# Optimization experiments

Hardware: AMD Instinct MI355X
Metric: run time of the kernel (lower is better)

The kernel has to match this reference:

```python
import jax, jax.numpy as jnp
import numpy as np

N = 50000
E = 1600000
D_IN = 128
HID = 64
OUT = 64
NEG_SLOPE = 0.2


def _glorot(key, shape):
    fan_in = shape[0]
    return jax.random.normal(key, shape, dtype=jnp.float32) / np.sqrt(fan_in)


def _layer_params(key, din, dout):
    ks = jax.random.split(key, 4)
    return dict(
        Wl=_glorot(ks[0], (din, dout)), bl=jnp.zeros((dout,), jnp.float32),
        Wr=_glorot(ks[1], (din, dout)), br=jnp.zeros((dout,), jnp.float32),
        We=_glorot(ks[2], (1, dout)),
        att=jax.random.normal(ks[3], (dout,), dtype=jnp.float32) / np.sqrt(dout),
        b=jnp.zeros((dout,), jnp.float32),
    )


def setup_inputs() -> dict:
    key = jax.random.key(0)
    kx, ke, ka, k0, k1, k2 = jax.random.split(key, 6)
    x = jax.random.normal(kx, (N, D_IN), dtype=jnp.float32)
    edge_index = jax.random.randint(ke, (2, E), 0, N, dtype=jnp.int64)
    edge_attr = jax.random.uniform(ka, (E, 1), dtype=jnp.float32)
    p0 = _layer_params(k0, D_IN, HID)
    p1 = _layer_params(k1, HID, HID)
    p2 = _layer_params(k2, HID, OUT)
    inp = {"x": x, "edge_index": edge_index, "edge_attr": edge_attr}
    for i, p in enumerate((p0, p1, p2)):
        for name, v in p.items():
            inp[f"{name}{i}"] = v
    return inp


def gatv2_layer(x, src, dst, edge_attr, Wl, bl, Wr, br, We, att, b):
    # GATv2Conv, heads=1, no self loops, edge_dim=1
    xl = x @ Wl + bl                      # [N, C] source transform
    xr = x @ Wr + br                      # [N, C] target transform
    m = xl[src] + xr[dst] + edge_attr @ We  # [E, C]
    m = jnp.where(m > 0, m, NEG_SLOPE * m)  # leaky_relu(0.2)
    logits = m @ att                      # [E]
    # segment softmax over destination nodes
    lmax = jax.ops.segment_max(logits, dst, num_segments=N)
    lmax = jnp.where(jnp.isfinite(lmax), lmax, 0.0)
    ex = jnp.exp(logits - lmax[dst])
    denom = jax.ops.segment_sum(ex, dst, num_segments=N)
    alpha = ex / (denom[dst] + 1e-16)     # [E]
    out = jax.ops.segment_sum(xl[src] * alpha[:, None], dst, num_segments=N)
    return out + b


def reference(x, edge_index, edge_attr,
              Wl0, bl0, Wr0, br0, We0, att0, b0,
              Wl1, bl1, Wr1, br1, We1, att1, b1,
              Wl2, bl2, Wr2, br2, We2, att2, b2):
    src, dst = edge_index[0], edge_index[1]
    h = gatv2_layer(x, src, dst, edge_attr, Wl0, bl0, Wr0, br0, We0, att0, b0)
    h = jax.nn.relu(h)
    h = gatv2_layer(h, src, dst, edge_attr, Wl1, bl1, Wr1, br1, We1, att1, b1)
    h = jax.nn.relu(h)
    h = gatv2_layer(h, src, dst, edge_attr, Wl2, bl2, Wr2, br2, We2, att2, b2)
    # final_activation=False
    return h
```

## Files before the change

### kernel.cpp

```cpp
#include <hip/hip_runtime.h>
#include <math.h>


#define NEG_SLOPE 0.2f

__global__ __launch_bounds__(256) void kA_hist(
    const int* __restrict__ dst, int E, int nbuck, int chunk,
    int* __restrict__ blockhist )
{
    __shared__ int h[256];
    int tid = threadIdx.x, blk = blockIdx.x, nblk = gridDim.x;
    for (int i = tid; i < nbuck; i += 256) h[i] = 0;
    __syncthreads();
    int s0 = blk * chunk, s1 = min(s0 + chunk, E);
    for (int e = s0 + tid; e < s1; e += 256)
        atomicAdd(&h[dst[e] >> 8], 1);
    __syncthreads();
    for (int i = tid; i < nbuck; i += 256)
        blockhist[i * nblk + blk] = h[i];
}

__global__ __launch_bounds__(1024) void k_scan(const int* __restrict__ counts, int n,
                                               int* __restrict__ offsets) {
    __shared__ int wsum[16];
    __shared__ int wpre[16];
    __shared__ int chunktot;
    int tid = threadIdx.x;
    int lane = tid & 63;
    int w = tid >> 6;
    int carry = 0;
    for (int base = 0; base < n; base += 1024) {
        int i = base + tid;
        int v = (i < n) ? counts[i] : 0;
        int incl = v;
        #pragma unroll
        for (int off = 1; off < 64; off <<= 1) {
            int t = __shfl_up(incl, off, 64);
            if (lane >= off) incl += t;
        }
        if (lane == 63) wsum[w] = incl;
        __syncthreads();
        if (tid == 0) {
            int acc = 0;
            #pragma unroll
            for (int j = 0; j < 16; ++j) { int t = wsum[j]; wpre[j] = acc; acc += t; }
            chunktot = acc;
        }
        __syncthreads();
        int excl = incl - v + wpre[w] + carry;
        if (i < n) offsets[i] = excl;
        carry += chunktot;
        __syncthreads();
    }
    if (tid == 0) offsets[n] = carry;
}

__global__ __launch_bounds__(256) void kA_scatter(
    const int* __restrict__ src, const int* __restrict__ dst,
    const float* __restrict__ ea, int E, int nbuck, int chunk, int nblk,
    const int* __restrict__ cursA, int2* __restrict__ tmp)
{
    __shared__ int cur[256];
    int tid = threadIdx.x, blk = blockIdx.x;
    for (int i = tid; i < nbuck; i += 256) cur[i] = cursA[i * nblk + blk];
    __syncthreads();
    int s0 = blk * chunk, s1 = min(s0 + chunk, E);
    for (int e = s0 + tid; e < s1; e += 256) {
        int d = dst[e];
        int pos = atomicAdd(&cur[d >> 8], 1);
        tmp[pos] = make_int2((d << 16) | src[e], __float_as_int(ea[e]));
    }
}

__global__ __launch_bounds__(256) void kB_sort(
    const int2* __restrict__ tmp, const int* __restrict__ cursA,
    int nblk, int E, int n,
    int2* __restrict__ srec, int* __restrict__ offsets)
{
    __shared__ int h[256];
    __shared__ int cur2[256];
    int b = blockIdx.x, tid = threadIdx.x;
    int start = cursA[b * nblk];
    int end   = cursA[(b + 1) * nblk];
    h[tid] = 0;
    __syncthreads();
    for (int e = start + tid; e < end; e += 256)
        atomicAdd(&h[(tmp[e].x >> 16) & 255], 1);
    __syncthreads();
    if (tid == 0) {
        int acc = start;
        for (int i = 0; i < 256; ++i) { int c = h[i]; cur2[i] = acc; acc += c; }
    }
    __syncthreads();
    int v = (b << 8) + tid;
    if (v < n) offsets[v] = cur2[tid];
    if (b == 0 && tid == 0) offsets[n] = E;
    __syncthreads();
    for (int e = start + tid; e < end; e += 256) {
        int2 r = tmp[e];
        int pos = atomicAdd(&cur2[(r.x >> 16) & 255], 1);
        srec[pos] = make_int2(r.x & 0xFFFF, r.y);
    }
}

template<int DIN>
__global__ __launch_bounds__(256) void k_linear(
    const float* __restrict__ x,
    const float* __restrict__ Wl, const float* __restrict__ bl,
    const float* __restrict__ Wr, const float* __restrict__ br,
    float* __restrict__ xl, float* __restrict__ xr, int n)
{
    __shared__ float sWl[DIN * 64];
    __shared__ float sWr[DIN * 64];
    __shared__ float sX[16 * DIN];
    int tid = threadIdx.x;
    for (int i = tid * 4; i < DIN * 64; i += 256 * 4) {
        *(float4*)&sWl[i] = *(const float4*)&Wl[i];
        *(float4*)&sWr[i] = *(const float4*)&Wr[i];
    }
    int nb = blockIdx.x * 16;
    int totx = n * DIN;
    for (int i = tid * 4; i < 16 * DIN; i += 256 * 4) {
        int g = nb * DIN + i;
        if (g < totx) *(float4*)&sX[i] = *(const float4*)&x[g];
    }
    __syncthreads();
    int lane = tid & 63;
    int grp = tid >> 6;
    float blv = bl[lane], brv = br[lane];
    float accL[4], accR[4];
    #pragma unroll
    for (int j = 0; j < 4; ++j) { accL[j] = blv; accR[j] = brv; }
    const float* sx0 = &sX[(grp * 4) * DIN];
    #pragma unroll 4
    for (int k = 0; k < DIN; ++k) {
        float wl = sWl[k * 64 + lane];
        float wr = sWr[k * 64 + lane];
        #pragma unroll
        for (int j = 0; j < 4; ++j) {
            float xk = sx0[j * DIN + k];
            accL[j] += xk * wl;
            accR[j] += xk * wr;
        }
    }
    #pragma unroll
    for (int j = 0; j < 4; ++j) {
        int node = nb + grp * 4 + j;
        if (node < n) {
            xl[node * 64 + lane] = accL[j];
            xr[node * 64 + lane] = accR[j];
        }
    }
}

__global__ __launch_bounds__(256) void k_edge(
    const float* __restrict__ xl, const float* __restrict__ xr,
    const int2* __restrict__ srec,
    const int* __restrict__ offsets,
    const float* __restrict__ We, const float* __restrict__ att,
    const float* __restrict__ b,
    float* __restrict__ out, int n, int relu)
{
    int wave = threadIdx.x >> 6;
    int lane = threadIdx.x & 63;
    int v = blockIdx.x * 4 + wave;
    if (v >= n) return;
    int start = offsets[v];
    int end   = offsets[v + 1];
    float xr_c  = xr[v * 64 + lane];
    float We_c  = We[lane];
    float att_c = att[lane];
    float M = -INFINITY, S = 0.f, O = 0.f;

    for (int e = start; e < end; e += 8) {
        int cnt = end - e;
        int2 rec[8]; float xlc[8], p[8];
        #pragma unroll
        for (int i = 0; i < 8; ++i) {
            int ii = (i < cnt) ? i : 0;
            rec[i] = srec[e + ii];
        }
        #pragma unroll
        for (int i = 0; i < 8; ++i) xlc[i] = xl[rec[i].x * 64 + lane];
        #pragma unroll
        for (int i = 0; i < 8; ++i) {
            float m = xlc[i] + xr_c + __int_as_float(rec[i].y) * We_c;
            m = m > 0.f ? m : NEG_SLOPE * m;
            p[i] = (i < cnt) ? m * att_c : -INFINITY;
        }
        float q[4];
        #pragma unroll
        for (int i = 0; i < 4; ++i) {
            float a = p[2*i]   + __shfl_xor(p[2*i],   1, 64);
            float c = p[2*i+1] + __shfl_xor(p[2*i+1], 1, 64);
            q[i] = (lane & 1) ? c : a;
        }
        float r[2];
        #pragma unroll
        for (int i = 0; i < 2; ++i) {
            float a = q[2*i]   + __shfl_xor(q[2*i],   2, 64);
            float c = q[2*i+1] + __shfl_xor(q[2*i+1], 2, 64);
            r[i] = (lane & 2) ? c : a;
        }
        float s_;
        {
            float a = r[0] + __shfl_xor(r[0], 4, 64);
            float c = r[1] + __shfl_xor(r[1], 4, 64);
            s_ = (lane & 4) ? c : a;
        }
        s_ += __shfl_xor(s_, 8, 64);
        s_ += __shfl_xor(s_, 16, 64);
        s_ += __shfl_xor(s_, 32, 64);

        float bm = s_;
        bm = fmaxf(bm, __shfl_xor(bm, 1, 64));
        bm = fmaxf(bm, __shfl_xor(bm, 2, 64));
        bm = fmaxf(bm, __shfl_xor(bm, 4, 64));

        float newM = fmaxf(M, bm);
        float scale = __expf(M - newM);
        float wv = __expf(s_ - newM);

        float w0 = __shfl(wv, 0, 64), w1 = __shfl(wv, 1, 64);
        float w2 = __shfl(wv, 2, 64), w3 = __shfl(wv, 3, 64);
        float w4 = __shfl(wv, 4, 64), w5 = __shfl(wv, 5, 64);
        float w6 = __shfl(wv, 6, 64), w7 = __shfl(wv, 7, 64);
        float sw = ((w0 + w1) + (w2 + w3)) + ((w4 + w5) + (w6 + w7));
        float ow = w0*xlc[0] + w1*xlc[1] + w2*xlc[2] + w3*xlc[3]
                 + w4*xlc[4] + w5*xlc[5] + w6*xlc[6] + w7*xlc[7];
        S = S * scale + sw;
        O = O * scale + ow;
        M = newM;
    }
    float res = O / (S + 1e-16f) + b[lane];
    if (relu) res = fmaxf(res, 0.f);
    out[v * 64 + lane] = res;
}

extern "C" void kernel_launch(void* const* d_in, const int* in_sizes, int n_in,
                              void* d_out, int out_size, void* d_ws, size_t ws_size,
                              hipStream_t stream)
{
    const float* x  = (const float*)d_in[0];
    const int*   ei = (const int*)d_in[1];
    const float* ea = (const float*)d_in[2];
    const int N = in_sizes[0] / 128;
    const int E = in_sizes[1] / 2;
    const int* src = ei;
    const int* dst = ei + E;

    const float* P[21];
    for (int i = 0; i < 21; ++i) P[i] = (const float*)d_in[3 + i];

    const int NBLK  = 256;
    const int nbuck = (N + 255) >> 8;
    const int chunk = (E + NBLK - 1) / NBLK;
    const int nscan = nbuck * NBLK;

    char* ws = (char*)d_ws;
    size_t off = 0;
    auto alloc = [&](size_t bytes) { char* p = ws + off; off += (bytes + 255) & ~255ULL; return p; };
    float* xl        = (float*)alloc((size_t)N * 64 * 4);
    float* xr        = (float*)alloc((size_t)N * 64 * 4);
    float* h0        = (float*)alloc((size_t)N * 64 * 4);
    float* h1        = (float*)alloc((size_t)N * 64 * 4);
    int2*  srec      = (int2*)alloc((size_t)E * 8);
    int*   blockhist = (int*)alloc((size_t)nscan * 4);
    int*   cursA     = (int*)alloc((size_t)(nscan + 1) * 4);
    int*   offsets   = (int*)alloc((size_t)(N + 1) * 4);
    int2*  tmp       = (int2*)h0;

    kA_hist   <<<NBLK, 256, 0, stream>>>(dst, E, nbuck, chunk, blockhist);
    k_scan    <<<1, 1024, 0, stream>>>(blockhist, nscan, cursA);
    kA_scatter<<<NBLK, 256, 0, stream>>>(src, dst, ea, E, nbuck, chunk, NBLK, cursA, tmp);
    kB_sort   <<<nbuck, 256, 0, stream>>>(tmp, cursA, NBLK, E, N, srec, offsets);

    const int lgrid = (N + 15) / 16;
    const int egrid = (N + 3) / 4;

    k_linear<128><<<lgrid, 256, 0, stream>>>(x, P[0], P[1], P[2], P[3], xl, xr, N);
    k_edge<<<egrid, 256, 0, stream>>>(xl, xr, srec, offsets, P[4], P[5], P[6], h0, N, 1);
    k_linear<64><<<lgrid, 256, 0, stream>>>(h0, P[7], P[8], P[9], P[10], xl, xr, N);
    k_edge<<<egrid, 256, 0, stream>>>(xl, xr, srec, offsets, P[11], P[12], P[13], h1, N, 1);
    k_linear<64><<<lgrid, 256, 0, stream>>>(h1, P[14], P[15], P[16], P[17], xl, xr, N);
    k_edge<<<egrid, 256, 0, stream>>>(xl, xr, srec, offsets, P[18], P[19], P[20], (float*)d_out, N, 0);
}
```

Baseline: 542.6 us.

## Process two nodes per wave with float2 channels in edge kernel

The edge aggregation kernel now splits each 64-lane wave into two 32-lane halves, each handling one destination node with two channels per lane loaded as float2. The aim is to keep more lanes busy on low-degree nodes, halve the per-node reduction and shuffle overhead, and issue wider gathers. The cost is some divergence when the two nodes in a wave have different degrees, since the loop runs to the longer one. There is also extra per-lane arithmetic for the two channels.

```diff
diff --git a/kernel.cpp b/kernel.cpp
--- a/kernel.cpp
+++ b/kernel.cpp
@@ -163,54 +163,65 @@
 {
     int wave = threadIdx.x >> 6;
     int lane = threadIdx.x & 63;
-    int v = blockIdx.x * 4 + wave;
-    if (v >= n) return;
-    int start = offsets[v];
-    int end   = offsets[v + 1];
-    float xr_c  = xr[v * 64 + lane];
-    float We_c  = We[lane];
-    float att_c = att[lane];
-    float M = -INFINITY, S = 0.f, O = 0.f;
+    int h    = lane >> 5;
+    int j    = lane & 31;
+    int v = blockIdx.x * 8 + wave * 2 + h;
+    bool valid = v < n;
+    int vv = valid ? v : n - 1;
+    int start = offsets[vv];
+    int end   = valid ? offsets[vv + 1] : start;
+
+    float2 xr_c  = *(const float2*)&xr[vv * 64 + 2 * j];
+    float2 We_c  = *(const float2*)&We[2 * j];
+    float2 att_c = *(const float2*)&att[2 * j];
+    float2 b_c   = *(const float2*)&b[2 * j];
+
+    float M = -INFINITY, S = 0.f;
+    float Ox = 0.f, Oy = 0.f;
 
     for (int e = start; e < end; e += 8) {
         int cnt = end - e;
-        int2 rec[8]; float xlc[8], p[8];
+        int2 rec[8]; float2 xlc[8]; float p[8];
         #pragma unroll
         for (int i = 0; i < 8; ++i) {
             int ii = (i < cnt) ? i : 0;
             rec[i] = srec[e + ii];
         }
         #pragma unroll
-        for (int i = 0; i < 8; ++i) xlc[i] = xl[rec[i].x * 64 + lane];
+        for (int i = 0; i < 8; ++i)
+            xlc[i] = *(const float2*)&xl[rec[i].x * 64 + 2 * j];
         #pragma unroll
         for (int i = 0; i < 8; ++i) {
-            float m = xlc[i] + xr_c + __int_as_float(rec[i].y) * We_c;
-            m = m > 0.f ? m : NEG_SLOPE * m;
-            p[i] = (i < cnt) ? m * att_c : -INFINITY;
+            float ea = __int_as_float(rec[i].y);
+            float zx = xlc[i].x + xr_c.x + ea * We_c.x;
+            float zy = xlc[i].y + xr_c.y + ea * We_c.y;
+            zx = fmaxf(zx, NEG_SLOPE * zx);
+            zy = fmaxf(zy, NEG_SLOPE * zy);
+            float pp = att_c.x * zx + att_c.y * zy;
+            p[i] = (i < cnt) ? pp : -INFINITY;
         }
         float q[4];
         #pragma unroll
         for (int i = 0; i < 4; ++i) {
             float a = p[2*i]   + __shfl_xor(p[2*i],   1, 64);
             float c = p[2*i+1] + __shfl_xor(p[2*i+1], 1, 64);
-            q[i] = (lane & 1) ? c : a;
+            q[i] = (j & 1) ? c : a;
         }
         float r[2];
         #pragma unroll
         for (int i = 0; i < 2; ++i) {
             float a = q[2*i]   + __shfl_xor(q[2*i],   2, 64);
             float c = q[2*i+1] + __shfl_xor(q[2*i+1], 2, 64);
-            r[i] = (lane & 2) ? c : a;
+            r[i] = (j & 2) ? c : a;
         }
         float s_;
         {
             float a = r[0] + __shfl_xor(r[0], 4, 64);
             float c = r[1] + __shfl_xor(r[1], 4, 64);
-            s_ = (lane & 4) ? c : a;
+            s_ = (j & 4) ? c : a;
         }
         s_ += __shfl_xor(s_, 8, 64);
         s_ += __shfl_xor(s_, 16, 64);
-        s_ += __shfl_xor(s_, 32, 64);
 
         float bm = s_;
         bm = fmaxf(bm, __shfl_xor(bm, 1, 64));
@@ -221,20 +232,28 @@
         float scale = __expf(M - newM);
         float wv = __expf(s_ - newM);
 
-        float w0 = __shfl(wv, 0, 64), w1 = __shfl(wv, 1, 64);
-        float w2 = __shfl(wv, 2, 64), w3 = __shfl(wv, 3, 64);
-        float w4 = __shfl(wv, 4, 64), w5 = __shfl(wv, 5, 64);
-        float w6 = __shfl(wv, 6, 64), w7 = __shfl(wv, 7, 64);
+        float w0 = __shfl(wv, 0, 32), w1 = __shfl(wv, 1, 32);
+        float w2 = __shfl(wv, 2, 32), w3 = __shfl(wv, 3, 32);
+        float w4 = __shfl(wv, 4, 32), w5 = __shfl(wv, 5, 32);
+        float w6 = __shfl(wv, 6, 32), w7 = __shfl(wv, 7, 32);
         float sw = ((w0 + w1) + (w2 + w3)) + ((w4 + w5) + (w6 + w7));
-        float ow = w0*xlc[0] + w1*xlc[1] + w2*xlc[2] + w3*xlc[3]
-                 + w4*xlc[4] + w5*xlc[5] + w6*xlc[6] + w7*xlc[7];
-        S = S * scale + sw;
-        O = O * scale + ow;
+        float owx = w0*xlc[0].x + w1*xlc[1].x + w2*xlc[2].x + w3*xlc[3].x
+                  + w4*xlc[4].x + w5*xlc[5].x + w6*xlc[6].x + w7*xlc[7].x;
+        float owy = w0*xlc[0].y + w1*xlc[1].y + w2*xlc[2].y + w3*xlc[3].y
+                  + w4*xlc[4].y + w5*xlc[5].y + w6*xlc[6].y + w7*xlc[7].y;
+        S  = S  * scale + sw;
+        Ox = Ox * scale + owx;
+        Oy = Oy * scale + owy;
         M = newM;
     }
-    float res = O / (S + 1e-16f) + b[lane];
-    if (relu) res = fmaxf(res, 0.f);
-    out[v * 64 + lane] = res;
+    float inv = 1.f / (S + 1e-16f);
+    float rx = Ox * inv + b_c.x;
+    float ry = Oy * inv + b_c.y;
+    if (relu) { rx = fmaxf(rx, 0.f); ry = fmaxf(ry, 0.f); }
+    if (valid) {
+        float2 res = make_float2(rx, ry);
+        *(float2*)&out[v * 64 + 2 * j] = res;
+    }
 }
 
 extern "C" void kernel_launch(void* const* d_in, const int* in_sizes, int n_in,
@@ -276,7 +295,7 @@
     kB_sort   <<<nbuck, 256, 0, stream>>>(tmp, cursA, NBLK, E, N, srec, offsets);
 
     const int lgrid = (N + 15) / 16;
-    const int egrid = (N + 3) / 4;
+    const int egrid = (N + 7) / 8;
 
     k_linear<128><<<lgrid, 256, 0, stream>>>(x, P[0], P[1], P[2], P[3], xl, xr, N);
     k_edge<<<egrid, 256, 0, stream>>>(xl, xr, srec, offsets, P[4], P[5], P[6], h0, N, 1);
```

Result: faster. 501.0 us (-7.7%).
